# Optimization experiments

Measured on AMD Instinct MI355X. Metric: run time of the kernel, lower is better.

## Reference

```python
import jax, jax.numpy as jnp
import numpy as np

EPS = 1e-4

def mp_weight(w):
    # MP_GeoLinear eval-mode weight: normalize then scale by gain/sqrt(fan_in)
    w32 = w.astype(jnp.float32)
    norm = jnp.linalg.norm(w32, axis=1, keepdims=True)          # [out,1]
    fan_in = w.shape[1]
    denom = EPS + norm / np.sqrt(fan_in)                        # torch.add(eps, norm, alpha=sqrt(1/fan_in))
    wn = w32 / denom
    return (wn / np.sqrt(fan_in)).astype(w.dtype)               # gain=1


def setup_inputs() -> dict:
    key = jax.random.key(0)
    k1, k2, k3, k4 = jax.random.split(key, 4)
    N, E, C = 100000, 1600000, 128
    x = jax.random.normal(k1, (N, C), dtype=jnp.float32)
    edge_index = jax.random.randint(k2, (2, E), 0, N, dtype=jnp.int64)
    w_neigh = jax.random.normal(k3, (C, C), dtype=jnp.float32)
    w_res = jax.random.normal(k4, (C, C), dtype=jnp.float32)
    return {"x": x, "edge_index": edge_index, "w_neigh": w_neigh, "w_res": w_res}


def reference(x, edge_index, w_neigh, w_res):
    N = x.shape[0]
    row, col = edge_index[0], edge_index[1]            # source, target
    # degree of target nodes
    deg = jax.ops.segment_sum(jnp.ones_like(col, dtype=x.dtype), col, num_segments=N)
    deg_inv = jnp.where(deg > 0, deg ** -0.5, 0.0)     # inf -> 0
    norm = deg_inv[col]                                 # [E]
    # message: x_j * norm, aggregate: scatter-add into col
    msg = x[row] * norm[:, None]                        # [E,C]
    agg = jax.ops.segment_sum(msg, col, num_segments=N) # [N,C]
    neighbourhood = agg @ mp_weight(w_neigh).T
    residual = x @ mp_weight(w_res).T
    # mp_sum(residual, neighbourhood, t=0.5) = (a+b)/sqrt(2)
    join = (residual + neighbourhood) / np.sqrt(2.0)
    out = jnp.where((deg > 0)[:, None], join, residual)
    return out
```

## Files before the change

kernel.cpp:

```cpp
#include <hip/hip_runtime.h>
#include <hip/hip_bf16.h>

#define C 128
#define INV_SQRT2 0.7071067811865476f
#define NB 1024
#define BS 128
#define EPB 4096
#define NXCD 8
#define SUBCAP 384
#define LIDX_CAP 4096
#define AGS 68

typedef __attribute__((ext_vector_type(8))) short short8;
typedef __attribute__((ext_vector_type(4))) float f32x4;

__device__ inline ushort f2b(float f) {
    __hip_bfloat16 h = __float2bfloat16(f);
    return __builtin_bit_cast(ushort, h);
}


__global__ __launch_bounds__(512) void k_front(
    const int* __restrict__ row, const int* __restrict__ col, int E, int nblk,
    int* __restrict__ gcursor, unsigned int* __restrict__ recs,
    const float4* __restrict__ x, ushort* __restrict__ xb, int n4, int castBlocks,
    const float* __restrict__ w_res, const float* __restrict__ w_neigh,
    ushort* __restrict__ Bp)
{
    __shared__ int hist[NB];
    __shared__ int lbase[NB];
    int b = blockIdx.x;
    int t = threadIdx.x;
    if (b < nblk) {
        hist[t] = 0; hist[t + 512] = 0;
        __syncthreads();
        int base = b * EPB;
        #pragma unroll
        for (int i = 0; i < EPB / 512; i++) {
            int e = base + i * 512 + t;
            if (e < E) atomicAdd(&hist[col[e] >> 7], 1);
        }
        __syncthreads();
        int xcd = b & 7;
        int* gc = gcursor + xcd * NB;
        #pragma unroll
        for (int kx = 0; kx < 2; kx++) {
            int bb = t + kx * 512;
            int h = hist[bb];
            lbase[bb] = h ? atomicAdd(&gc[bb], h) : 0;
        }
        __syncthreads();
        hist[t] = 0; hist[t + 512] = 0;
        __syncthreads();
        #pragma unroll
        for (int i = 0; i < EPB / 512; i++) {
            int e = base + i * 512 + t;
            if (e < E) {
                int c = col[e];
                int kk = c >> 7;
                int p = atomicAdd(&hist[kk], 1) + lbase[kk];
                if (p < SUBCAP)
                    recs[((size_t)kk * NXCD + xcd) * SUBCAP + p] =
                        ((unsigned int)(c & 127) << 24) | (unsigned int)row[e];
            }
        }
    } else if (b < nblk + castBlocks) {
        int i = (b - nblk) * 512 + t;
        if (i < n4) {
            float4 v = x[i];
            ushort4 o;
            o.x = f2b(v.x); o.y = f2b(v.y); o.z = f2b(v.z); o.w = f2b(v.w);
            *(ushort4*)(xb + (size_t)i * 4) = o;
        }
        if (b == nblk && t < 32) {
            ushort4 z = make_ushort4(0, 0, 0, 0);
            *(ushort4*)(xb + ((size_t)n4 << 2) + (t << 2)) = z;
        }
    } else {
        int r = (b - nblk - castBlocks) * 8 + (t >> 6);
        int h = r >> 7;
        int i = r & 127;
        const float* w = h ? w_neigh : w_res;
        int lane = t & 63;
        float a = w[i * C + lane];
        float bb = w[i * C + lane + 64];
        float ss = a * a + bb * bb;
        #pragma unroll
        for (int off = 32; off > 0; off >>= 1) ss += __shfl_down(ss, off);
        ss = __shfl(ss, 0);
        float norm = sqrtf(ss);
        float denom = 1e-4f + norm * 0.08838834764831845f;
        float scale = 1.0f / (denom * 11.313708498984761f);
        int c1 = lane, c2 = lane + 64;
        Bp[(size_t)(h * 16 + (c1 >> 3)) * 1024 + i * 8 + (c1 & 7)] = f2b(a * scale);
        Bp[(size_t)(h * 16 + (c2 >> 3)) * 1024 + i * 8 + (c2 & 7)] = f2b(bb * scale);
    }
}


#define ACCUM(v) do { \
    acc[0] += __builtin_bit_cast(float, (v).x << 16); \
    acc[1] += __builtin_bit_cast(float, (v).x & 0xffff0000u); \
    acc[2] += __builtin_bit_cast(float, (v).y << 16); \
    acc[3] += __builtin_bit_cast(float, (v).y & 0xffff0000u); \
    acc[4] += __builtin_bit_cast(float, (v).z << 16); \
    acc[5] += __builtin_bit_cast(float, (v).z & 0xffff0000u); \
    acc[6] += __builtin_bit_cast(float, (v).w << 16); \
    acc[7] += __builtin_bit_cast(float, (v).w & 0xffff0000u); \
} while (0)

__global__ __launch_bounds__(512, 8) void k_fused(
    const unsigned int* __restrict__ recs, const int* __restrict__ gcursor,
    const ushort* __restrict__ xb, const ushort* __restrict__ Bp,
    int* __restrict__ lidxg, float* __restrict__ out, int N)
{
    __shared__ int shist[BS];
    __shared__ int sexcl[BS];
    __shared__ int scur[BS];
    __shared__ int scnt[NXCD];
    __shared__ uint sAgg[BS * AGS];

    int k = blockIdx.x;
    int t = threadIdx.x;
    const unsigned int* rb = recs + (size_t)k * NXCD * SUBCAP;
    int* lw = lidxg + (size_t)k * LIDX_CAP;

    if (t < NXCD) {
        int c = gcursor[t * NB + k];
        scnt[t] = (c > SUBCAP) ? SUBCAP : c;
    }
    if (t < BS) shist[t] = 0;
    __syncthreads();
    #pragma unroll 1
    for (int x = 0; x < NXCD; x++) {
        int cx = scnt[x];
        for (int i = t; i < cx; i += 512)
            atomicAdd(&shist[rb[x * SUBCAP + i] >> 24], 1);
    }
    __syncthreads();
    if (t < 64) {
        int a = shist[t], b = shist[t + 64];
        int pa = (a + 7) & ~7, pb = (b + 7) & ~7;
        int ia = pa, ib = pb;
        #pragma unroll
        for (int off = 1; off < 64; off <<= 1) {
            int ya = __shfl_up(ia, off);
            int yb = __shfl_up(ib, off);
            if (t >= off) { ia += ya; ib += yb; }
        }
        int tot0 = __shfl(ia, 63);
        int e0 = ia - pa;
        int e1 = ib - pb + tot0;
        sexcl[t] = e0;      scur[t] = e0;
        sexcl[t + 64] = e1; scur[t + 64] = e1;
    }
    __syncthreads();
    #pragma unroll 1
    for (int x = 0; x < NXCD; x++) {
        int cx = scnt[x];
        for (int i = t; i < cx; i += 512) {
            unsigned int r = rb[x * SUBCAP + i];
            int c = r >> 24;
            int p = atomicAdd(&scur[c], 1);
            lw[p] = (int)(r & 0xFFFFFF);
        }
    }
    if (t < BS) {
        int d = shist[t], b0 = sexcl[t];
        int pe = b0 + ((d + 7) & ~7);
        for (int p = b0 + d; p < pe; p++) lw[p] = N;
    }
    __syncthreads();

    int lane = t & 63;
    int wave = t >> 6;
    int s  = lane >> 4;
    int cl = lane & 15;
    const ushort* xcl = xb + (cl << 3);
    #pragma unroll 1
    for (int ln = wave * 16; ln < wave * 16 + 16; ln++) {
        int j  = sexcl[ln];
        int d  = shist[ln];
        int jend = j + ((d + 7) & ~7);
        float acc[8];
        #pragma unroll
        for (int i = 0; i < 8; i++) acc[i] = 0.f;
        for (; j + 16 <= jend; j += 16) {
            int i0 = lw[j + s];
            int i1 = lw[j + 4 + s];
            int i2 = lw[j + 8 + s];
            int i3 = lw[j + 12 + s];
            uint4 va = *(const uint4*)(xcl + ((size_t)i0 << 7));
            uint4 vb = *(const uint4*)(xcl + ((size_t)i1 << 7));
            uint4 vc = *(const uint4*)(xcl + ((size_t)i2 << 7));
            uint4 vd = *(const uint4*)(xcl + ((size_t)i3 << 7));
            ACCUM(va);
            ACCUM(vb);
            ACCUM(vc);
            ACCUM(vd);
        }
        if (j < jend) {
            int i0 = lw[j + s];
            int i1 = lw[j + 4 + s];
            uint4 va = *(const uint4*)(xcl + ((size_t)i0 << 7));
            uint4 vb = *(const uint4*)(xcl + ((size_t)i1 << 7));
            ACCUM(va);
            ACCUM(vb);
        }
        #pragma unroll
        for (int i = 0; i < 8; i++) {
            acc[i] += __shfl_xor(acc[i], 16);
            acc[i] += __shfl_xor(acc[i], 32);
        }
        float dd = (d > 0) ? rsqrtf((float)d) : 0.f;
        if (lane < 16) {
            uint4 o;
            o.x = (uint)f2b(acc[0] * dd) | ((uint)f2b(acc[1] * dd) << 16);
            o.y = (uint)f2b(acc[2] * dd) | ((uint)f2b(acc[3] * dd) << 16);
            o.z = (uint)f2b(acc[4] * dd) | ((uint)f2b(acc[5] * dd) << 16);
            o.w = (uint)f2b(acc[6] * dd) | ((uint)f2b(acc[7] * dd) << 16);
            *(uint4*)&sAgg[ln * AGS + cl * 4] = o;
        }
    }
    asm volatile("s_waitcnt lgkmcnt(0)" ::: "memory");

    int quad = lane >> 4;
    int l16  = lane & 15;
    long gbase = (long)k * BS;
    int arow = wave * 16 + l16;
    long garow = gbase + arow;
    if (garow >= N) garow = N - 1;

    f32x4 oacc[8];
    #pragma unroll
    for (int nt = 0; nt < 8; nt++) oacc[nt] = (f32x4){0.f, 0.f, 0.f, 0.f};

    #pragma unroll
    for (int kk = 0; kk < 8; kk++) {
        short8 af;
        if (kk < 4) {
            af = *(const short8*)(xb + garow * C + kk * 32 + quad * 8);
        } else {
            af = *(const short8*)&sAgg[arow * AGS + (kk - 4) * 16 + quad * 4];
        }
        #pragma unroll
        for (int nt = 0; nt < 8; nt++) {
            short8 bf = *(const short8*)(Bp +
                ((size_t)((kk * 4 + quad) * 128) + nt * 16 + l16) * 8);
            oacc[nt] = __builtin_amdgcn_mfma_f32_16x16x32_bf16(af, bf, oacc[nt], 0, 0, 0);
        }
    }

    #pragma unroll
    for (int r2 = 0; r2 < 4; r2++) {
        int rl = wave * 16 + quad * 4 + r2;
        long rowg = gbase + rl;
        if (rowg < N) {
            float sc = (shist[rl] > 0) ? INV_SQRT2 : 1.0f;
            float* o = out + rowg * C + l16;
            #pragma unroll
            for (int nt = 0; nt < 8; nt++)
                __builtin_nontemporal_store(oacc[nt][r2] * sc, &o[nt * 16]);
        }
    }
}


extern "C" void kernel_launch(void* const* d_in, const int* in_sizes, int n_in,
                              void* d_out, int out_size, void* d_ws, size_t ws_size,
                              hipStream_t stream) {
    const float* x       = (const float*)d_in[0];
    const int*   eidx    = (const int*)d_in[1];
    const float* w_neigh = (const float*)d_in[2];
    const float* w_res   = (const float*)d_in[3];
    float* out = (float*)d_out;

    int N = in_sizes[0] / C;
    int E = in_sizes[1] / 2;
    const int* row = eidx;
    const int* col = eidx + E;

    char* ws = (char*)d_ws;
    size_t off = 0;
    auto alloc = [&](size_t bytes) {
        size_t o = off;
        off += (bytes + 511) & ~(size_t)511;
        return o;
    };
    int nblk = (E + EPB - 1) / EPB;

    int*    gcursor    = (int*)(ws + alloc((size_t)NXCD * NB * 4));
    unsigned int* recs = (unsigned int*)(ws + alloc((size_t)NB * NXCD * SUBCAP * 4));
    ushort* Bp         = (ushort*)(ws + alloc((size_t)32 * 1024 * 2));
    ushort* xb         = (ushort*)(ws + alloc((size_t)N * C * 2 + 65536));
    int*    lidxg      = (int*)(ws + alloc((size_t)NB * LIDX_CAP * 4));
    (void)ws_size;

    hipMemsetAsync(gcursor, 0, (size_t)NXCD * NB * 4, stream);

    int nbuckets = (N + BS - 1) / BS;
    int n4 = N * C / 4;
    int castBlocks = (n4 + 511) / 512;

    k_front<<<nblk + castBlocks + 32, 512, 0, stream>>>(
        row, col, E, nblk, gcursor, recs,
        (const float4*)x, xb, n4, castBlocks, w_res, w_neigh, Bp);
    k_fused<<<nbuckets, 512, 0, stream>>>(recs, gcursor, xb, Bp, lidxg, out, N);
}
```

Before: 210.9 us.

## Single-pass edge binning, padded global cursors, coarser cast blocks, split fused launch

The front kernel now reads col/row only once: it takes each edge's local rank in the bucket histogram in the first pass and keeps the record and key in registers, removing the second histogram pass and its global reload. Global bucket cursors are padded by a stride of 16 ints, which spreads the atomic counters onto separate cache lines. The cast loop has each block convert four float4 chunks, cutting the number of blocks. The fused kernel is launched as two half grids, which adds one launch and may hurt tail overlap.

```diff
diff --git a/kernel.cpp b/kernel.cpp
--- a/kernel.cpp
+++ b/kernel.cpp
@@ -10,6 +10,7 @@
 #define SUBCAP 384
 #define LIDX_CAP 4096
 #define AGS 68
+#define GSTRIDE 16
 
 typedef __attribute__((ext_vector_type(8))) short short8;
 typedef __attribute__((ext_vector_type(4))) float f32x4;
@@ -32,45 +33,55 @@
     int b = blockIdx.x;
     int t = threadIdx.x;
     if (b < nblk) {
+        unsigned int rec0[EPB / 512];
+        unsigned int key0[EPB / 512];
         hist[t] = 0; hist[t + 512] = 0;
         __syncthreads();
         int base = b * EPB;
-        #pragma unroll
-        for (int i = 0; i < EPB / 512; i++) {
-            int e = base + i * 512 + t;
-            if (e < E) atomicAdd(&hist[col[e] >> 7], 1);
-        }
-        __syncthreads();
-        int xcd = b & 7;
-        int* gc = gcursor + xcd * NB;
-        #pragma unroll
-        for (int kx = 0; kx < 2; kx++) {
-            int bb = t + kx * 512;
-            int h = hist[bb];
-            lbase[bb] = h ? atomicAdd(&gc[bb], h) : 0;
-        }
-        __syncthreads();
-        hist[t] = 0; hist[t + 512] = 0;
-        __syncthreads();
         #pragma unroll
         for (int i = 0; i < EPB / 512; i++) {
             int e = base + i * 512 + t;
             if (e < E) {
                 int c = col[e];
                 int kk = c >> 7;
-                int p = atomicAdd(&hist[kk], 1) + lbase[kk];
+                int r = atomicAdd(&hist[kk], 1);
+                rec0[i] = ((unsigned int)(c & 127) << 24) | (unsigned int)row[e];
+                key0[i] = (unsigned int)kk | ((unsigned int)r << 10);
+            } else {
+                key0[i] = 0xFFFFFFFFu;
+            }
+        }
+        __syncthreads();
+        int xcd = b & 7;
+        int* gc = gcursor + (size_t)xcd * NB * GSTRIDE;
+        #pragma unroll
+        for (int kx = 0; kx < 2; kx++) {
+            int bb = t + kx * 512;
+            int h = hist[bb];
+            lbase[bb] = h ? atomicAdd(&gc[bb * GSTRIDE], h) : 0;
+        }
+        __syncthreads();
+        #pragma unroll
+        for (int i = 0; i < EPB / 512; i++) {
+            unsigned int key = key0[i];
+            if (key != 0xFFFFFFFFu) {
+                int kk = (int)(key & 1023u);
+                int p = lbase[kk] + (int)(key >> 10);
                 if (p < SUBCAP)
-                    recs[((size_t)kk * NXCD + xcd) * SUBCAP + p] =
-                        ((unsigned int)(c & 127) << 24) | (unsigned int)row[e];
+                    recs[((size_t)kk * NXCD + xcd) * SUBCAP + p] = rec0[i];
             }
         }
     } else if (b < nblk + castBlocks) {
-        int i = (b - nblk) * 512 + t;
-        if (i < n4) {
-            float4 v = x[i];
-            ushort4 o;
-            o.x = f2b(v.x); o.y = f2b(v.y); o.z = f2b(v.z); o.w = f2b(v.w);
-            *(ushort4*)(xb + (size_t)i * 4) = o;
+        int i0 = (b - nblk) * 2048 + t;
+        #pragma unroll
+        for (int u = 0; u < 4; u++) {
+            int i = i0 + u * 512;
+            if (i < n4) {
+                float4 v = x[i];
+                ushort4 o;
+                o.x = f2b(v.x); o.y = f2b(v.y); o.z = f2b(v.z); o.w = f2b(v.w);
+                *(ushort4*)(xb + (size_t)i * 4) = o;
+            }
         }
         if (b == nblk && t < 32) {
             ushort4 z = make_ushort4(0, 0, 0, 0);
@@ -112,35 +123,35 @@
 __global__ __launch_bounds__(512, 8) void k_fused(
     const unsigned int* __restrict__ recs, const int* __restrict__ gcursor,
     const ushort* __restrict__ xb, const ushort* __restrict__ Bp,
-    int* __restrict__ lidxg, float* __restrict__ out, int N)
+    int* __restrict__ lidxg, float* __restrict__ out, int N, int kofs)
 {
     __shared__ int shist[BS];
     __shared__ int sexcl[BS];
     __shared__ int scur[BS];
-    __shared__ int scnt[NXCD];
+    __shared__ int scnt8[NXCD];
     __shared__ uint sAgg[BS * AGS];
 
-    int k = blockIdx.x;
+    int k = blockIdx.x + kofs;
     int t = threadIdx.x;
     const unsigned int* rb = recs + (size_t)k * NXCD * SUBCAP;
     int* lw = lidxg + (size_t)k * LIDX_CAP;
 
     if (t < NXCD) {
-        int c = gcursor[t * NB + k];
-        scnt[t] = (c > SUBCAP) ? SUBCAP : c;
+        int c0 = gcursor[((size_t)t * NB + k) * GSTRIDE];
+        scnt8[t] = (c0 > SUBCAP) ? SUBCAP : c0;
     }
     if (t < BS) shist[t] = 0;
     __syncthreads();
     #pragma unroll 1
-    for (int x = 0; x < NXCD; x++) {
-        int cx = scnt[x];
+    for (int xx = 0; xx < NXCD; xx++) {
+        int cx = scnt8[xx];
         for (int i = t; i < cx; i += 512)
-            atomicAdd(&shist[rb[x * SUBCAP + i] >> 24], 1);
+            atomicAdd(&shist[rb[xx * SUBCAP + i] >> 24], 1);
     }
     __syncthreads();
     if (t < 64) {
-        int a = shist[t], b = shist[t + 64];
-        int pa = (a + 7) & ~7, pb = (b + 7) & ~7;
+        int a = shist[t], bb = shist[t + 64];
+        int pa = (a + 7) & ~7, pb = (bb + 7) & ~7;
         int ia = pa, ib = pb;
         #pragma unroll
         for (int off = 1; off < 64; off <<= 1) {
@@ -156,10 +167,10 @@
     }
     __syncthreads();
     #pragma unroll 1
-    for (int x = 0; x < NXCD; x++) {
-        int cx = scnt[x];
+    for (int xx = 0; xx < NXCD; xx++) {
+        int cx = scnt8[xx];
         for (int i = t; i < cx; i += 512) {
-            unsigned int r = rb[x * SUBCAP + i];
+            unsigned int r = rb[xx * SUBCAP + i];
             int c = r >> 24;
             int p = atomicAdd(&scur[c], 1);
             lw[p] = (int)(r & 0xFFFFFF);
@@ -289,21 +300,26 @@
     };
     int nblk = (E + EPB - 1) / EPB;
 
-    int*    gcursor    = (int*)(ws + alloc((size_t)NXCD * NB * 4));
+    int*    gcursor    = (int*)(ws + alloc((size_t)NXCD * NB * GSTRIDE * 4));
     unsigned int* recs = (unsigned int*)(ws + alloc((size_t)NB * NXCD * SUBCAP * 4));
     ushort* Bp         = (ushort*)(ws + alloc((size_t)32 * 1024 * 2));
     ushort* xb         = (ushort*)(ws + alloc((size_t)N * C * 2 + 65536));
     int*    lidxg      = (int*)(ws + alloc((size_t)NB * LIDX_CAP * 4));
     (void)ws_size;
 
-    hipMemsetAsync(gcursor, 0, (size_t)NXCD * NB * 4, stream);
+    hipMemsetAsync(gcursor, 0, (size_t)NXCD * NB * GSTRIDE * 4, stream);
 
     int nbuckets = (N + BS - 1) / BS;
     int n4 = N * C / 4;
-    int castBlocks = (n4 + 511) / 512;
+    int castBlocks = (n4 + 2047) / 2048;
 
     k_front<<<nblk + castBlocks + 32, 512, 0, stream>>>(
         row, col, E, nblk, gcursor, recs,
         (const float4*)x, xb, n4, castBlocks, w_res, w_neigh, Bp);
-    k_fused<<<nbuckets, 512, 0, stream>>>(recs, gcursor, xb, Bp, lidxg, out, N);
+
+    int half = (nbuckets + 1) / 2;
+    k_fused<<<half, 512, 0, stream>>>(recs, gcursor, xb, Bp, lidxg, out, N, 0);
+    if (nbuckets - half > 0)
+        k_fused<<<nbuckets - half, 512, 0, stream>>>(recs, gcursor, xb, Bp, lidxg,
+                                                     out, N, half);
 }
```

New measurement: 225.7 us. +7.1%, slower.
